# Optimization experiments

Measured on AMD Instinct MI355X. Metric: run time of the kernel, lower is better.

Reference implementation:

```python
import jax, jax.numpy as jnp
import numpy as np

B, C, H, W = 2, 48, 128, 256
HEADS = 3
EPS_LN = 1e-6
EPS_NRM = 1e-12


def _conv(x, w, b, padding=0, dilation=1, groups=1):
    # x: NCHW, w: OIHW
    out = jax.lax.conv_general_dilated(
        x, w, window_strides=(1, 1),
        padding=[(padding, padding), (padding, padding)],
        rhs_dilation=(dilation, dilation),
        feature_group_count=groups,
        dimension_numbers=('NCHW', 'OIHW', 'NCHW'))
    return out + b[None, :, None, None]


def _ln2d(x, w, b):
    # LayerNorm over channel dim per pixel (NAFNet-style LayerNorm2d)
    mu = x.mean(axis=1, keepdims=True)
    var = ((x - mu) ** 2).mean(axis=1, keepdims=True)
    return (x - mu) / jnp.sqrt(var + EPS_LN) * w[None, :, None, None] + b[None, :, None, None]


def _l2norm(x):
    # F.normalize(dim=-1): x / max(||x||_2, eps)
    n = jnp.sqrt((x * x).sum(-1, keepdims=True))
    return x / jnp.maximum(n, EPS_NRM)


def setup_inputs() -> dict:
    key = jax.random.key(0)
    ks = iter(jax.random.split(key, 40))
    def nrm(shape, s=0.02):
        return jax.random.normal(next(ks), shape, jnp.float32) * s
    d = {
        'x_l': jax.random.normal(next(ks), (B, C, H, W), jnp.float32),
        'x_r': jax.random.normal(next(ks), (B, C, H, W), jnp.float32),
        'ln1_w': jnp.ones((C,), jnp.float32), 'ln1_b': jnp.zeros((C,), jnp.float32),
        'ln2_w': jnp.ones((C,), jnp.float32), 'ln2_b': jnp.zeros((C,), jnp.float32),
        'qkv_l_w': nrm((3 * C, C, 1, 1)), 'qkv_l_b': jnp.zeros((3 * C,), jnp.float32),
        'qkv_r_w': nrm((3 * C, C, 1, 1)), 'qkv_r_b': jnp.zeros((3 * C,), jnp.float32),
        'dw_l_w': nrm((3 * C, 1, 3, 3)), 'dw_l_b': jnp.zeros((3 * C,), jnp.float32),
        'dw_r_w': nrm((3 * C, 1, 3, 3)), 'dw_r_b': jnp.zeros((3 * C,), jnp.float32),
        'dil0_w': nrm((2 * C, 2 * C, 3, 3)), 'dil0_b': jnp.zeros((2 * C,), jnp.float32),
        'dil1_w': nrm((2 * C, 2 * C, 3, 3)), 'dil1_b': jnp.zeros((2 * C,), jnp.float32),
        'dil2_w': nrm((2 * C, 2 * C, 3, 3)), 'dil2_b': jnp.zeros((2 * C,), jnp.float32),
        'convQ_w': nrm((C, 6 * C, 1, 1)), 'convQ_b': jnp.zeros((C,), jnp.float32),
        'conv1_w': nrm((C, C, 1, 1)), 'conv1_b': jnp.zeros((C,), jnp.float32),
        'conv2_w': nrm((C, C, 1, 1)), 'conv2_b': jnp.zeros((C,), jnp.float32),
        'temperature': jnp.ones((HEADS, 1, 1), jnp.float32),
    }
    return d


def reference(x_l, x_r, ln1_w, ln1_b, ln2_w, ln2_b,
              qkv_l_w, qkv_l_b, qkv_r_w, qkv_r_b,
              dw_l_w, dw_l_b, dw_r_w, dw_r_b,
              dil0_w, dil0_b, dil1_w, dil1_b, dil2_w, dil2_b,
              convQ_w, convQ_b, conv1_w, conv1_b, conv2_w, conv2_b,
              temperature):
    b, c, h, w = x_l.shape
    hw = h * w
    ch = c // HEADS  # channels per head

    norm_l = _ln2d(x_l, ln1_w, ln1_b)
    norm_r = _ln2d(x_r, ln2_w, ln2_b)

    qkvl = _conv(_conv(norm_l, qkv_l_w, qkv_l_b), dw_l_w, dw_l_b, padding=1, groups=3 * c)
    qkvr = _conv(_conv(norm_r, qkv_r_w, qkv_r_b), dw_r_w, dw_r_b, padding=1, groups=3 * c)
    Q_l, K_l, V_l = jnp.split(qkvl, 3, axis=1)
    Q_r, K_r, V_r = jnp.split(qkvr, 3, axis=1)

    Q = jnp.concatenate((Q_l, Q_r), axis=1)  # [b, 2c, h, w]
    Q = jnp.concatenate((
        _conv(Q, dil0_w, dil0_b, padding=2, dilation=2),
        _conv(Q, dil1_w, dil1_b, padding=4, dilation=4),
        _conv(Q, dil2_w, dil2_b, padding=6, dilation=6)), axis=1)  # [b, 6c, h, w]
    Q = _conv(Q, convQ_w, convQ_b)  # [b, c, h, w]

    def heads(t):
        return t.reshape(b, HEADS, ch, hw)

    Q = _l2norm(heads(Q))
    K_l = _l2norm(heads(K_l))
    K_r = _l2norm(heads(K_r))
    V_l = heads(V_l)
    V_r = heads(V_r)

    # channel attention: [b, head, ch, ch]
    A_r2l = jax.nn.softmax(jnp.einsum('bhcn,bhdn->bhcd', Q, K_r) * temperature, axis=-1)
    A_l2r = jax.nn.softmax(jnp.einsum('bhcn,bhdn->bhcd', Q, K_l) * temperature, axis=-1)

    F_l = jnp.einsum('bhcd,bhdn->bhcn', A_r2l, V_l).reshape(b, c, h, w)
    F_r = jnp.einsum('bhcd,bhdn->bhcn', A_l2r, V_r).reshape(b, c, h, w)

    F_l = _conv(F_l, conv1_w, conv1_b)
    F_r = _conv(F_r, conv2_w, conv2_b)
    return (x_l + F_l, x_r + F_r)
```

## Files before the change

### kernel.cpp

```cpp
#include <hip/hip_runtime.h>
#include <hip/hip_bf16.h>

typedef __hip_bfloat16 bf16;
typedef __attribute__((ext_vector_type(8))) short short8;
typedef __attribute__((ext_vector_type(4))) float f32x4;

constexpr int IMG_H = 128;
constexpr int IMG_W = 256;
constexpr int HW    = IMG_H * IMG_W;
constexpr int BB    = 2;
constexpr int CC    = 48;
constexpr int C3    = 144;
constexpr int XPW   = 268;
constexpr int XOFF  = 6;

constexpr int WO_QKVL_W = 0;
constexpr int WO_QKVR_W = 6912;
constexpr int WO_DWL_W  = 13824;
constexpr int WO_DWR_W  = 15120;
constexpr int WO_C1_W   = 16416;
constexpr int WO_C2_W   = 18720;
constexpr int WO_QKVL_B = 21024;
constexpr int WO_QKVR_B = 21168;
constexpr int WO_DWL_B  = 21312;
constexpr int WO_DWR_B  = 21456;
constexpr int WO_C1_B   = 21600;
constexpr int WO_C2_B   = 21648;
constexpr int WO_LN1W   = 21696;
constexpr int WO_LN1B   = 21744;
constexpr int WO_LN2W   = 21792;
constexpr int WO_LN2B   = 21840;
constexpr int WO_TEMP   = 21888;
constexpr int WO_WQ     = 21952;
constexpr int WO_D0W    = 35776;
constexpr int WO_D1W    = 118720;
constexpr int WO_D2W    = 201664;
constexpr int WO_BQ     = 284608;
constexpr int WO_B0     = 284656;
constexpr int WO_B1     = 284752;
constexpr int WO_B2     = 284848;
constexpr int WO_WPACK  = 284944;
constexpr int WO_EFFB   = 409360;
constexpr int WO_NQ     = 409424;
constexpr int WO_NKL    = 409520;
constexpr int WO_NKR    = 409616;
constexpr int WO_AR2L   = 409712;
constexpr int WO_AL2R   = 411248;
constexpr int WO_M1     = 412800;
constexpr int WO_M2     = 417408;
constexpr int WO_WQP    = 422016;
constexpr int WO_PART   = 431232;

constexpr size_t ACT_BASE_BYTES = 2118144;

constexpr size_t A_P  = 0;
constexpr size_t A_Q1 = 9437184;
constexpr size_t A_Q2 = 18874368;
constexpr size_t A_QC = 28311552;

struct PrepArgs {
  const void* src[25];
  int dst[25];
  int n[25];
};

__device__ __forceinline__ bool probe_bf16(const void* ln1w) {
  return ((const unsigned short*)ln1w)[0] == 0x3F80;
}

__global__ __launch_bounds__(256) void prep_k(PrepArgs a, float* __restrict__ wsf) {
  bool isb = probe_bf16(a.src[12]);
  int t = blockIdx.y;
  int i = blockIdx.x * 256 + threadIdx.x;
  if (i < a.n[t]) {
    float v = isb ? __bfloat162float(((const bf16*)a.src[t])[i])
                  : ((const float*)a.src[t])[i];
    wsf[a.dst[t] + i] = v;
  }
}

__global__ __launch_bounds__(256) void effw2_k(const float* __restrict__ wsf,
                                               bf16* __restrict__ wpack) {
  int d  = blockIdx.x / 96;
  int ci = blockIdx.x % 96;
  __shared__ float wds[864];
  __shared__ float wqs[48 * 97];
  const int wdb = (d == 0) ? WO_D0W : (d == 1) ? WO_D1W : WO_D2W;
  for (int idx = threadIdx.x; idx < 864; idx += 256) {
    int m = idx / 9, tt = idx % 9;
    wds[idx] = wsf[wdb + (m * 96 + ci) * 9 + tt];
  }
  for (int idx = threadIdx.x; idx < 4608; idx += 256) {
    int co = idx / 96, m = idx % 96;
    wqs[co * 97 + m] = wsf[WO_WQ + co * 288 + d * 96 + m];
  }
  __syncthreads();
  int tco = threadIdx.x;
  if (tco < 432) {
    int t = tco / 48, co = tco % 48;
    float s = 0.f;
#pragma unroll 8
    for (int m = 0; m < 96; ++m) s += wqs[co * 97 + m] * wds[m * 9 + t];
    int kc = ci >> 5, j = ci & 7;
    int L = ((ci & 31) >> 3) * 16 + (co & 15);
    int nt = co >> 4;
    int f = ((d * 9 + t) * 3 + kc) * 3 + nt;
    wpack[(size_t)f * 512 + L * 8 + j] = __float2bfloat16(s);
  }
}

__global__ __launch_bounds__(64) void effb_k(const float* __restrict__ wsf,
                                             float* __restrict__ effb) {
  int co = threadIdx.x;
  if (co >= 48) return;
  float s = wsf[WO_BQ + co];
  for (int m = 0; m < 96; ++m) {
    s += wsf[WO_WQ + co * 288 + m]       * wsf[WO_B0 + m];
    s += wsf[WO_WQ + co * 288 + 96 + m]  * wsf[WO_B1 + m];
    s += wsf[WO_WQ + co * 288 + 192 + m] * wsf[WO_B2 + m];
  }
  effb[co] = s;
}

__global__ __launch_bounds__(256) void wqp_k(const float* __restrict__ wsf,
                                             bf16* __restrict__ wqp) {
  int idx = blockIdx.x * 256 + threadIdx.x;
  if (idx >= 18432) return;
  int side = idx / 9216;
  int rem = idx % 9216;
  int nt = rem / 1024;
  int kt = (rem / 512) % 2;
  int e  = rem % 512;
  int L = e >> 3, j = e & 7;
  int o = nt * 16 + (L & 15);
  int kp = kt * 32 + (L >> 4) * 8 + j;
  int g = kp >> 4, r = kp & 15;
  float val = 0.f;
  if (r < 12) {
    int c = g * 12 + r;
    val = wsf[(side ? WO_QKVR_W : WO_QKVL_W) + o * 48 + c];
  }
  wqp[idx] = __float2bfloat16(val);
}

__global__ __launch_bounds__(256) void ln_k(
    const void* __restrict__ x, const void* __restrict__ probe,
    const float* __restrict__ lnw, const float* __restrict__ lnb,
    bf16* __restrict__ xn) {
  int px = threadIdx.x & 63;
  int w  = threadIdx.x >> 6;
  int p  = blockIdx.x * 64 + px;
  int b  = p >> 15;
  int pix = p & (HW - 1);
  size_t base = (size_t)b * CC * HW + pix;
  float v[12];
  if (probe_bf16(probe)) {
    const bf16* xp = (const bf16*)x + base;
#pragma unroll
    for (int c = 0; c < 12; ++c)
      v[c] = __bfloat162float(xp[(size_t)(w * 12 + c) * HW]);
  } else {
    const float* xp = (const float*)x + base;
#pragma unroll
    for (int c = 0; c < 12; ++c) v[c] = xp[(size_t)(w * 12 + c) * HW];
  }
  float s = 0.f, s2 = 0.f;
#pragma unroll
  for (int c = 0; c < 12; ++c) { s += v[c]; s2 += v[c] * v[c]; }
  __shared__ float2 red[4][64];
  red[w][px] = make_float2(s, s2);
  __syncthreads();
  float S = 0.f, S2 = 0.f;
#pragma unroll
  for (int i = 0; i < 4; ++i) { S += red[i][px].x; S2 += red[i][px].y; }
  float mu = S * (1.f / 48.f);
  float var = S2 * (1.f / 48.f) - mu * mu;
  float rs = rsqrtf(var + 1e-6f);
  bf16 o[16];
#pragma unroll
  for (int c = 0; c < 12; ++c)
    o[c] = __float2bfloat16((v[c] - mu) * rs * lnw[w * 12 + c] + lnb[w * 12 + c]);
#pragma unroll
  for (int c = 12; c < 16; ++c) o[c] = __float2bfloat16(0.f);
  bf16* dst = xn + (size_t)p * 64 + w * 16;
  *(uint4*)(dst) = *(uint4*)(o);
  *(uint4*)(dst + 8) = *(uint4*)(o + 8);
}

__global__ __launch_bounds__(256) void qkv_mfma_k(
    const bf16* __restrict__ xn, const bf16* __restrict__ wqp_side,
    const float* __restrict__ qb, bf16* __restrict__ pre) {
  __shared__ __align__(16) bf16 W[18 * 512];
  __shared__ __align__(16) bf16 Cs[144][72];
  for (int i = threadIdx.x; i < 1152; i += 256)
    ((uint4*)W)[i] = ((const uint4*)wqp_side)[i];
  __syncthreads();
  int L = threadIdx.x & 63, w = threadIdx.x >> 6;
  int lo = L & 15, hi = L >> 4;
  int p0 = blockIdx.x * 64 + w * 16;
  const bf16* abase = xn + (size_t)(p0 + lo) * 64 + hi * 8;
  short8 a0 = *(const short8*)(abase);
  short8 a1 = *(const short8*)(abase + 32);
#pragma unroll
  for (int nt = 0; nt < 9; ++nt) {
    float bv = qb[nt * 16 + lo];
    f32x4 acc = {bv, bv, bv, bv};
    acc = __builtin_amdgcn_mfma_f32_16x16x32_bf16(
        a0, *(const short8*)(W + (nt * 2 + 0) * 512 + L * 8), acc, 0, 0, 0);
    acc = __builtin_amdgcn_mfma_f32_16x16x32_bf16(
        a1, *(const short8*)(W + (nt * 2 + 1) * 512 + L * 8), acc, 0, 0, 0);
#pragma unroll
    for (int r = 0; r < 4; ++r)
      Cs[nt * 16 + lo][w * 16 + hi * 4 + r] = __float2bfloat16(acc[r]);
  }
  __syncthreads();
  int b = (blockIdx.x * 64) >> 15;
  int pix0 = (blockIdx.x * 64) & (HW - 1);
#pragma unroll
  for (int pass = 0; pass < 18; ++pass) {
    int o = pass * 8 + (threadIdx.x >> 5);
    int px = (threadIdx.x & 31) * 2;
    bf16 t2[2];
    t2[0] = Cs[o][px];
    t2[1] = Cs[o][px + 1];
    *(unsigned*)(pre + ((size_t)(b * C3 + o)) * HW + pix0 + px) = *(unsigned*)t2;
  }
}

__global__ __launch_bounds__(256) void dw_k(
    const bf16* __restrict__ in, const float* __restrict__ w9,
    const float* __restrict__ bias, bf16* __restrict__ out) {
  int gid = blockIdx.x;
  int yt = gid & 15;
  int c = (gid >> 4) % C3;
  int b = gid / (16 * C3);
  int ry = threadIdx.x >> 5, xi = threadIdx.x & 31;
  int y = yt * 8 + ry;
  int x0 = xi * 8;
  const bf16* base = in + ((size_t)(b * C3 + c)) * HW;
  float wv[9];
#pragma unroll
  for (int t = 0; t < 9; ++t) wv[t] = w9[c * 9 + t];
  float bz = bias[c];
  float acc[8];
#pragma unroll
  for (int i = 0; i < 8; ++i) acc[i] = bz;
#pragma unroll
  for (int ky = 0; ky < 3; ++ky) {
    int yy = y + ky - 1;
    if ((unsigned)yy >= (unsigned)IMG_H) continue;
    const bf16* row = base + yy * IMG_W + x0;
    uint4 m = *(const uint4*)(row);
    float f[10];
    f[0] = (x0 > 0) ? __bfloat162float(row[-1]) : 0.f;
    f[9] = (x0 + 8 < IMG_W) ? __bfloat162float(row[8]) : 0.f;
    f[1] = __uint_as_float(m.x << 16);
    f[2] = __uint_as_float(m.x & 0xFFFF0000u);
    f[3] = __uint_as_float(m.y << 16);
    f[4] = __uint_as_float(m.y & 0xFFFF0000u);
    f[5] = __uint_as_float(m.z << 16);
    f[6] = __uint_as_float(m.z & 0xFFFF0000u);
    f[7] = __uint_as_float(m.w << 16);
    f[8] = __uint_as_float(m.w & 0xFFFF0000u);
    float w0 = wv[ky * 3], w1 = wv[ky * 3 + 1], w2 = wv[ky * 3 + 2];
#pragma unroll
    for (int i = 0; i < 8; ++i)
      acc[i] += w0 * f[i] + w1 * f[i + 1] + w2 * f[i + 2];
  }
  bf16 o[8];
#pragma unroll
  for (int i = 0; i < 8; ++i) o[i] = __float2bfloat16(acc[i]);
  *(uint4*)(out + ((size_t)(b * C3 + c)) * HW + y * IMG_W + x0) = *(uint4*)o;
}

__global__ __launch_bounds__(256) void qc_k(const bf16* __restrict__ q1,
                                            const bf16* __restrict__ q2,
                                            bf16* __restrict__ qc) {
  int b = blockIdx.x >> 7;
  int y = blockIdx.x & 127;
  int half = blockIdx.y;
  int tid = threadIdx.x;
  int x0 = half * 128;
  int px = tid & 127;
  int cig = tid >> 7;
  __shared__ __align__(16) bf16 T[128][100];
#pragma unroll 8
  for (int k = 0; k < 48; ++k) {
    int ci = cig * 48 + k;
    const bf16* src = (ci < 48)
        ? q1 + (((size_t)(b * C3 + ci)) * IMG_H + y) * IMG_W
        : q2 + (((size_t)(b * C3 + ci - 48)) * IMG_H + y) * IMG_W;
    T[px][ci] = src[x0 + px];
  }
  __syncthreads();
  size_t rowbase = ((size_t)(b * IMG_H + y)) * XPW * 96 + (size_t)half * 12864;
#pragma unroll 1
  for (int i = 0; i < 13; ++i) {
    int e4 = i * 256 + tid;
    if (e4 >= 3216) break;
    int e = e4 * 4;
    int xp = (e + half * 12864) / 96;
    int ci = (e + half * 12864) % 96;
    int x = xp - XOFF;
    uint2 val;
    if ((unsigned)x < (unsigned)IMG_W) {
      val = *(const uint2*)(&T[x - x0][ci]);
    } else {
      val.x = 0u; val.y = 0u;
    }
    *(uint2*)(qc + rowbase + e) = val;
  }
}

__global__ __launch_bounds__(256) void dil_mfma_k(
    const bf16* __restrict__ qc, const bf16* __restrict__ wp,
    const float* __restrict__ effb, bf16* __restrict__ qh) {
  __shared__ __align__(16) unsigned char LDSU[26304];
  bf16* Wb = (bf16*)LDSU;
  float* Cs = (float*)LDSU;
  int tid = threadIdx.x;
  int L = tid & 63;
  int w = tid >> 6;
  int lo = L & 15, hi = L >> 4;
  int x0 = blockIdx.x * 128;
  int y = blockIdx.y;
  int b = blockIdx.z;

  f32x4 acc[2][3];
#pragma unroll
  for (int s = 0; s < 2; ++s)
#pragma unroll
    for (int nt = 0; nt < 3; ++nt) {
      float bv = effb[nt * 16 + lo];
      acc[s][nt] = {bv, bv, bv, bv};
    }

  const size_t abase =
      ((size_t)(b * IMG_H + y) * XPW + XOFF + x0 + w * 32 + lo) * 96 + hi * 8;

  {
    const uint4* src = (const uint4*)(wp);
    uint4* dst = (uint4*)(Wb);
    dst[tid] = src[tid];
    dst[tid + 256] = src[tid + 256];
    if (tid < 64) dst[tid + 512] = src[tid + 512];
  }
  __syncthreads();

#pragma unroll 1
  for (int ti = 0; ti < 27; ++ti) {
    if (ti + 1 < 27) {
      const uint4* src = (const uint4*)(wp + (ti + 1) * 4608);
      uint4* dst = (uint4*)(Wb + ((ti + 1) & 1) * 4608);
      dst[tid] = src[tid];
      dst[tid + 256] = src[tid + 256];
      if (tid < 64) dst[tid + 512] = src[tid + 512];
    }
    int d = ti / 9, t = ti - d * 9;
    int D = 2 * (d + 1);
    int dy = (t / 3 - 1) * D;
    int dx = (t % 3 - 1) * D;
    int yy = y + dy;
    if ((unsigned)yy < (unsigned)IMG_H) {
      const bf16* wb = Wb + (ti & 1) * 4608 + L * 8;
      const bf16* ap = qc + abase + ((long)dy * XPW + dx) * 96;
#pragma unroll
      for (int kc = 0; kc < 3; ++kc) {
        short8 a0 = *(const short8*)(ap + kc * 32);
        short8 a1 = *(const short8*)(ap + kc * 32 + 1536);
        const bf16* wk = wb + kc * 3 * 512;
#pragma unroll
        for (int nt = 0; nt < 3; ++nt) {
          short8 wv = *(const short8*)(wk + nt * 512);
          acc[0][nt] = __builtin_amdgcn_mfma_f32_16x16x32_bf16(
              a0, wv, acc[0][nt], 0, 0, 0);
          acc[1][nt] = __builtin_amdgcn_mfma_f32_16x16x32_bf16(
              a1, wv, acc[1][nt], 0, 0, 0);
        }
      }
    }
    __syncthreads();
  }

#pragma unroll
  for (int s = 0; s < 2; ++s)
#pragma unroll
    for (int nt = 0; nt < 3; ++nt)
#pragma unroll
      for (int r = 0; r < 4; ++r)
        Cs[(nt * 16 + lo) * 137 + w * 32 + s * 16 + hi * 4 + r] = acc[s][nt][r];
  __syncthreads();
#pragma unroll
  for (int it = 0; it < 3; ++it) {
    int e = (it * 256 + tid) * 8;
    int co = e >> 7;
    int px = e & 127;
    const float* srcp = &Cs[co * 137 + px];
    bf16 tmp[8];
#pragma unroll
    for (int i2 = 0; i2 < 8; ++i2) tmp[i2] = __float2bfloat16(srcp[i2]);
    *(uint4*)(qh + (((size_t)(b * CC + co)) * IMG_H + y) * IMG_W + x0 + px) =
        *(uint4*)tmp;
  }
}

__device__ __forceinline__ float wave_sum(float v) {
#pragma unroll
  for (int off = 32; off > 0; off >>= 1) v += __shfl_down(v, off, 64);
  return v;
}

__device__ __forceinline__ float blo(unsigned u) {
  return __uint_as_float(u << 16);
}
__device__ __forceinline__ float bhi(unsigned u) {
  return __uint_as_float(u & 0xFFFF0000u);
}

__global__ __launch_bounds__(256) void rownorm_k(
    const bf16* __restrict__ qh, const bf16* __restrict__ qkvl,
    const bf16* __restrict__ qkvr, float* __restrict__ nq,
    float* __restrict__ nkl, float* __restrict__ nkr) {
  int id = blockIdx.x;
  int which = id / 96;
  int rid = id % 96;
  int b = rid / 48;
  int c = rid % 48;
  const bf16* ptr = (which == 0) ? qh + ((size_t)(b * CC + c)) * HW
                  : (which == 1) ? qkvl + ((size_t)(b * C3 + 48 + c)) * HW
                                 : qkvr + ((size_t)(b * C3 + 48 + c)) * HW;
  float s = 0.f;
#pragma unroll 2
  for (int it = 0; it < 16; ++it) {
    int n0 = (it * 256 + threadIdx.x) * 8;
    uint4 u = *(const uint4*)(ptr + n0);
    float a0 = blo(u.x), a1 = bhi(u.x), a2 = blo(u.y), a3 = bhi(u.y);
    float a4 = blo(u.z), a5 = bhi(u.z), a6 = blo(u.w), a7 = bhi(u.w);
    s += a0 * a0 + a1 * a1 + a2 * a2 + a3 * a3 + a4 * a4 + a5 * a5 +
         a6 * a6 + a7 * a7;
  }
  s = wave_sum(s);
  __shared__ float red[4];
  if ((threadIdx.x & 63) == 0) red[threadIdx.x >> 6] = s;
  __syncthreads();
  if (threadIdx.x == 0) {
    float tot = red[0] + red[1] + red[2] + red[3];
    float* dst = (which == 0) ? nq : (which == 1) ? nkl : nkr;
    dst[rid] = tot;
  }
}

__global__ __launch_bounds__(256) void logits_mfma_k(
    const bf16* __restrict__ qh, const bf16* __restrict__ qkvl,
    const bf16* __restrict__ qkvr, float* __restrict__ part) {
  int abh = blockIdx.x;
  int chunk = blockIdx.y;
  int a = abh / 6;
  int b = (abh / 3) % 2;
  int h = abh % 3;
  int tid = threadIdx.x;
  int L = tid & 63, w = tid >> 6;
  int lo = L & 15, hi = L >> 4;
  const bf16* qrow = qh + ((size_t)(b * CC + h * 16 + lo)) * HW;
  const bf16* krow =
      ((a == 0) ? qkvr : qkvl) + ((size_t)(b * C3 + 48 + h * 16 + lo)) * HW;
  int px0 = chunk * 1024 + w * 256 + hi * 8;
  f32x4 acc = {0.f, 0.f, 0.f, 0.f};
#pragma unroll
  for (int s = 0; s < 8; ++s) {
    short8 av = *(const short8*)(qrow + px0 + s * 32);
    short8 bv = *(const short8*)(krow + px0 + s * 32);
    acc = __builtin_amdgcn_mfma_f32_16x16x32_bf16(av, bv, acc, 0, 0, 0);
  }
  __shared__ float red[4][256];
#pragma unroll
  for (int r = 0; r < 4; ++r) red[w][(hi * 4 + r) * 16 + lo] = acc[r];
  __syncthreads();
  float sum = red[0][tid] + red[1][tid] + red[2][tid] + red[3][tid];
  part[((size_t)abh * 32 + chunk) * 256 + tid] = sum;
}

__global__ __launch_bounds__(256) void logits_red_k(
    const float* __restrict__ part, const float* __restrict__ nq,
    const float* __restrict__ nkl, const float* __restrict__ nkr,
    const float* __restrict__ temp, float* __restrict__ logr2l,
    float* __restrict__ logl2r) {
  int abh = blockIdx.x;
  int a = abh / 6, b = (abh / 3) % 2, h = abh % 3;
  int t = threadIdx.x;
  int i = t >> 4, j = t & 15;
  float s = 0.f;
  const float* p = part + (size_t)abh * 32 * 256 + t;
#pragma unroll 8
  for (int c = 0; c < 32; ++c) s += p[c * 256];
  float qn = fmaxf(sqrtf(nq[b * 48 + h * 16 + i]), 1e-12f);
  float kn = fmaxf(sqrtf(((a == 0) ? nkr : nkl)[b * 48 + h * 16 + j]), 1e-12f);
  float val = s / (qn * kn) * temp[h];
  ((a == 0) ? logr2l : logl2r)[b * 768 + h * 256 + i * 16 + j] = val;
}

__global__ __launch_bounds__(256) void softmaxM_k(float* __restrict__ wsf) {
  int tid = threadIdx.x;
  __shared__ float A1[1536], A2[1536];
  if (tid < 192) {
    const float* p = wsf + ((tid < 96) ? WO_AR2L : WO_AL2R) + (tid % 96) * 16;
    float* dst = ((tid < 96) ? A1 : A2) + (tid % 96) * 16;
    float m = -1e30f;
#pragma unroll
    for (int j = 0; j < 16; ++j) m = fmaxf(m, p[j]);
    float s = 0.f;
    float e[16];
#pragma unroll
    for (int j = 0; j < 16; ++j) {
      e[j] = expf(p[j] - m);
      s += e[j];
    }
    float inv = 1.f / s;
#pragma unroll
    for (int j = 0; j < 16; ++j) dst[j] = e[j] * inv;
  }
  __syncthreads();
#pragma unroll 1
  for (int idx = tid; idx < 4608; idx += 256) {
    int b = idx / 2304;
    int r = idx % 2304;
    int o = r / 48;
    int cp = r % 48;
    int h = cp >> 4, j = cp & 15;
    const float* a1 = &A1[((b * 3 + h) * 16) * 16 + j];
    const float* a2 = &A2[((b * 3 + h) * 16) * 16 + j];
    float s1 = 0.f, s2 = 0.f;
#pragma unroll
    for (int i = 0; i < 16; ++i) {
      s1 += wsf[WO_C1_W + o * 48 + h * 16 + i] * a1[i * 16];
      s2 += wsf[WO_C2_W + o * 48 + h * 16 + i] * a2[i * 16];
    }
    wsf[WO_M1 + idx] = s1;
    wsf[WO_M2 + idx] = s2;
  }
}

__global__ __launch_bounds__(256) void attn_out2_k(
    const bf16* __restrict__ qkv, const void* __restrict__ x,
    const void* __restrict__ probe, const float* __restrict__ M,
    const float* __restrict__ cb, void* __restrict__ out, int half) {
  int tid = threadIdx.x;
  int p = blockIdx.x * 256 + tid;
  int b = __builtin_amdgcn_readfirstlane(p >> 15);
  int pix = p & (HW - 1);
  int o0 = blockIdx.y * 16;
  bool isb = probe_bf16(probe);

  float v[CC];
  const bf16* vb = qkv + ((size_t)(b * C3 + 96)) * HW + pix;
#pragma unroll
  for (int c = 0; c < CC; ++c) v[c] = __bfloat162float(vb[(size_t)c * HW]);

  const float* Mb = M + b * 2304;
  size_t base = (size_t)b * CC * HW + pix;
  float res[16];
#pragma unroll 2
  for (int o = 0; o < 16; ++o) {
    float acc = cb[o0 + o];
    const float* mrow = Mb + (o0 + o) * 48;
#pragma unroll
    for (int c = 0; c < CC; ++c) acc += mrow[c] * v[c];
    res[o] = acc;
  }
  size_t obase = (size_t)half * BB * CC * HW + base + (size_t)o0 * HW;
  if (isb) {
    const bf16* xp = (const bf16*)x + base + (size_t)o0 * HW;
    bf16* op = (bf16*)out + obase;
#pragma unroll
    for (int o = 0; o < 16; ++o)
      op[(size_t)o * HW] =
          __float2bfloat16(res[o] + __bfloat162float(xp[(size_t)o * HW]));
  } else {
    const float* xp = (const float*)x + base + (size_t)o0 * HW;
    float* op = (float*)out + obase;
#pragma unroll
    for (int o = 0; o < 16; ++o) op[(size_t)o * HW] = res[o] + xp[(size_t)o * HW];
  }
}

extern "C" void kernel_launch(void* const* d_in, const int* in_sizes, int n_in,
                              void* d_out, int out_size, void* d_ws, size_t ws_size,
                              hipStream_t stream) {
  (void)in_sizes; (void)n_in; (void)out_size; (void)ws_size;
  const void* x_l = d_in[0];
  const void* x_r = d_in[1];
  const void* probe = d_in[2];
  float* wsf = (float*)d_ws;
  bf16* wpack = (bf16*)(wsf + WO_WPACK);
  bf16* wqp = (bf16*)(wsf + WO_WQP);
  bf16* act = (bf16*)((char*)d_ws + ACT_BASE_BYTES);
  bf16* P  = act + A_P;
  bf16* Q1 = act + A_Q1;
  bf16* Q2 = act + A_Q2;
  bf16* QC = act + A_QC;
  bf16* XN = act + A_QC;
  bf16* qh = P;

  PrepArgs pa;
  const int srcIdx[25] = {6, 8, 10, 12, 22, 24, 7, 9, 11, 13, 23, 25,
                          2, 3, 4, 5, 26, 20, 14, 16, 18, 21, 15, 17, 19};
  const int dstOff[25] = {WO_QKVL_W, WO_QKVR_W, WO_DWL_W, WO_DWR_W, WO_C1_W, WO_C2_W,
                          WO_QKVL_B, WO_QKVR_B, WO_DWL_B, WO_DWR_B, WO_C1_B, WO_C2_B,
                          WO_LN1W, WO_LN1B, WO_LN2W, WO_LN2B, WO_TEMP,
                          WO_WQ, WO_D0W, WO_D1W, WO_D2W, WO_BQ, WO_B0, WO_B1, WO_B2};
  const int ns[25] = {6912, 6912, 1296, 1296, 2304, 2304, 144, 144, 144, 144,
                      48, 48, 48, 48, 48, 48, 3,
                      13824, 82944, 82944, 82944, 48, 96, 96, 96};
  for (int i = 0; i < 25; ++i) {
    pa.src[i] = d_in[srcIdx[i]];
    pa.dst[i] = dstOff[i];
    pa.n[i] = ns[i];
  }
  prep_k<<<dim3(324, 25), 256, 0, stream>>>(pa, wsf);

  effw2_k<<<288, 256, 0, stream>>>(wsf, wpack);
  effb_k<<<1, 64, 0, stream>>>(wsf, wsf + WO_EFFB);
  wqp_k<<<72, 256, 0, stream>>>(wsf, wqp);

  ln_k<<<1024, 256, 0, stream>>>(x_l, probe, wsf + WO_LN1W, wsf + WO_LN1B, XN);
  qkv_mfma_k<<<1024, 256, 0, stream>>>(XN, wqp, wsf + WO_QKVL_B, P);
  dw_k<<<BB * C3 * 16, 256, 0, stream>>>(P, wsf + WO_DWL_W, wsf + WO_DWL_B, Q1);
  ln_k<<<1024, 256, 0, stream>>>(x_r, probe, wsf + WO_LN2W, wsf + WO_LN2B, XN);
  qkv_mfma_k<<<1024, 256, 0, stream>>>(XN, wqp + 9216, wsf + WO_QKVR_B, P);
  dw_k<<<BB * C3 * 16, 256, 0, stream>>>(P, wsf + WO_DWR_W, wsf + WO_DWR_B, Q2);

  qc_k<<<dim3(BB * IMG_H, 2), 256, 0, stream>>>(Q1, Q2, QC);

  dil_mfma_k<<<dim3(IMG_W / 128, IMG_H, BB), 256, 0, stream>>>(
      QC, wpack, wsf + WO_EFFB, qh);

  rownorm_k<<<288, 256, 0, stream>>>(qh, Q1, Q2, wsf + WO_NQ,
                                     wsf + WO_NKL, wsf + WO_NKR);
  logits_mfma_k<<<dim3(12, 32), 256, 0, stream>>>(qh, Q1, Q2, wsf + WO_PART);
  logits_red_k<<<12, 256, 0, stream>>>(wsf + WO_PART, wsf + WO_NQ,
                                       wsf + WO_NKL, wsf + WO_NKR,
                                       wsf + WO_TEMP, wsf + WO_AR2L,
                                       wsf + WO_AL2R);
  softmaxM_k<<<1, 256, 0, stream>>>(wsf);

  attn_out2_k<<<dim3(256, 3), 256, 0, stream>>>(
      Q1, x_l, probe, wsf + WO_M1, wsf + WO_C1_B, d_out, 0);
  attn_out2_k<<<dim3(256, 3), 256, 0, stream>>>(
      Q2, x_r, probe, wsf + WO_M2, wsf + WO_C2_B, d_out, 1);
}
```

Baseline: 294.0 us.

## Fuse layernorm into QKV MFMA, re-tile dilated conv by channel group, merge attn_out launches

```diff
diff --git a/kernel.cpp b/kernel.cpp
--- a/kernel.cpp
+++ b/kernel.cpp
@@ -101,10 +101,14 @@
     float s = 0.f;
 #pragma unroll 8
     for (int m = 0; m < 96; ++m) s += wqs[co * 97 + m] * wds[m * 9 + t];
+    int trow = t / 3, dxi = t % 3;
+    int ti = (trow == 0) ? (2 - d) * 3 + dxi
+           : (trow == 1) ? 9 + d * 3 + dxi
+                         : 18 + d * 3 + dxi;
     int kc = ci >> 5, j = ci & 7;
     int L = ((ci & 31) >> 3) * 16 + (co & 15);
     int nt = co >> 4;
-    int f = ((d * 9 + t) * 3 + kc) * 3 + nt;
+    int f = (ti * 3 + kc) * 3 + nt;
     wpack[(size_t)f * 512 + L * 8 + j] = __float2bfloat16(s);
   }
 }
@@ -143,14 +147,24 @@
   wqp[idx] = __float2bfloat16(val);
 }
 
-__global__ __launch_bounds__(256) void ln_k(
+__global__ __launch_bounds__(256) void lnqkv_k(
     const void* __restrict__ x, const void* __restrict__ probe,
     const float* __restrict__ lnw, const float* __restrict__ lnb,
-    bf16* __restrict__ xn) {
-  int px = threadIdx.x & 63;
-  int w  = threadIdx.x >> 6;
-  int p  = blockIdx.x * 64 + px;
-  int b  = p >> 15;
+    const bf16* __restrict__ wqp_side, const float* __restrict__ qb,
+    bf16* __restrict__ pre) {
+  __shared__ __align__(16) unsigned char LDSU[21504 + 18432];
+  bf16* XNs = (bf16*)LDSU;
+  float2* red = (float2*)(LDSU + 9216);
+  bf16* Cs = (bf16*)LDSU;
+  bf16* W = (bf16*)(LDSU + 21504);
+  int tid = threadIdx.x;
+  for (int i = tid; i < 1152; i += 256)
+    ((uint4*)W)[i] = ((const uint4*)wqp_side)[i];
+
+  int px = tid & 63;
+  int w = tid >> 6;
+  int p = blockIdx.x * 64 + px;
+  int b = p >> 15;
   int pix = p & (HW - 1);
   size_t base = (size_t)b * CC * HW + pix;
   float v[12];
@@ -167,63 +181,55 @@
   float s = 0.f, s2 = 0.f;
 #pragma unroll
   for (int c = 0; c < 12; ++c) { s += v[c]; s2 += v[c] * v[c]; }
-  __shared__ float2 red[4][64];
-  red[w][px] = make_float2(s, s2);
+  red[w * 64 + px] = make_float2(s, s2);
   __syncthreads();
   float S = 0.f, S2 = 0.f;
 #pragma unroll
-  for (int i = 0; i < 4; ++i) { S += red[i][px].x; S2 += red[i][px].y; }
+  for (int i = 0; i < 4; ++i) {
+    float2 r2 = red[i * 64 + px];
+    S += r2.x; S2 += r2.y;
+  }
   float mu = S * (1.f / 48.f);
   float var = S2 * (1.f / 48.f) - mu * mu;
   float rs = rsqrtf(var + 1e-6f);
-  bf16 o[16];
+  bf16 o16[16];
 #pragma unroll
   for (int c = 0; c < 12; ++c)
-    o[c] = __float2bfloat16((v[c] - mu) * rs * lnw[w * 12 + c] + lnb[w * 12 + c]);
-#pragma unroll
-  for (int c = 12; c < 16; ++c) o[c] = __float2bfloat16(0.f);
-  bf16* dst = xn + (size_t)p * 64 + w * 16;
-  *(uint4*)(dst) = *(uint4*)(o);
-  *(uint4*)(dst + 8) = *(uint4*)(o + 8);
-}
-
-__global__ __launch_bounds__(256) void qkv_mfma_k(
-    const bf16* __restrict__ xn, const bf16* __restrict__ wqp_side,
-    const float* __restrict__ qb, bf16* __restrict__ pre) {
-  __shared__ __align__(16) bf16 W[18 * 512];
-  __shared__ __align__(16) bf16 Cs[144][72];
-  for (int i = threadIdx.x; i < 1152; i += 256)
-    ((uint4*)W)[i] = ((const uint4*)wqp_side)[i];
-  __syncthreads();
-  int L = threadIdx.x & 63, w = threadIdx.x >> 6;
+    o16[c] = __float2bfloat16((v[c] - mu) * rs * lnw[w * 12 + c] + lnb[w * 12 + c]);
+#pragma unroll
+  for (int c = 12; c < 16; ++c) o16[c] = __float2bfloat16(0.f);
+  *(uint4*)(XNs + px * 72 + w * 16) = *(uint4*)(o16);
+  *(uint4*)(XNs + px * 72 + w * 16 + 8) = *(uint4*)(o16 + 8);
+  __syncthreads();
+
+  int L = tid & 63;
   int lo = L & 15, hi = L >> 4;
-  int p0 = blockIdx.x * 64 + w * 16;
-  const bf16* abase = xn + (size_t)(p0 + lo) * 64 + hi * 8;
-  short8 a0 = *(const short8*)(abase);
-  short8 a1 = *(const short8*)(abase + 32);
+  const bf16* arow = XNs + (size_t)(w * 16 + lo) * 72 + hi * 8;
+  short8 a0 = *(const short8*)(arow);
+  short8 a1 = *(const short8*)(arow + 32);
+  __syncthreads();
 #pragma unroll
   for (int nt = 0; nt < 9; ++nt) {
-    float bv = qb[nt * 16 + lo];
-    f32x4 acc = {bv, bv, bv, bv};
+    float bvv = qb[nt * 16 + lo];
+    f32x4 acc = {bvv, bvv, bvv, bvv};
     acc = __builtin_amdgcn_mfma_f32_16x16x32_bf16(
         a0, *(const short8*)(W + (nt * 2 + 0) * 512 + L * 8), acc, 0, 0, 0);
     acc = __builtin_amdgcn_mfma_f32_16x16x32_bf16(
         a1, *(const short8*)(W + (nt * 2 + 1) * 512 + L * 8), acc, 0, 0, 0);
 #pragma unroll
     for (int r = 0; r < 4; ++r)
-      Cs[nt * 16 + lo][w * 16 + hi * 4 + r] = __float2bfloat16(acc[r]);
-  }
-  __syncthreads();
-  int b = (blockIdx.x * 64) >> 15;
+      Cs[(nt * 16 + lo) * 66 + w * 16 + hi * 4 + r] = __float2bfloat16(acc[r]);
+  }
+  __syncthreads();
   int pix0 = (blockIdx.x * 64) & (HW - 1);
 #pragma unroll
   for (int pass = 0; pass < 18; ++pass) {
-    int o = pass * 8 + (threadIdx.x >> 5);
-    int px = (threadIdx.x & 31) * 2;
+    int o = pass * 8 + (tid >> 5);
+    int px2 = (tid & 31) * 2;
     bf16 t2[2];
-    t2[0] = Cs[o][px];
-    t2[1] = Cs[o][px + 1];
-    *(unsigned*)(pre + ((size_t)(b * C3 + o)) * HW + pix0 + px) = *(unsigned*)t2;
+    t2[0] = Cs[o * 66 + px2];
+    t2[1] = Cs[o * 66 + px2 + 1];
+    *(unsigned*)(pre + ((size_t)(b * C3 + o)) * HW + pix0 + px2) = *(unsigned*)t2;
   }
 }
 
@@ -312,70 +318,66 @@
   }
 }
 
-__global__ __launch_bounds__(256) void dil_mfma_k(
+__global__ __launch_bounds__(128) void dil_mfma_k(
     const bf16* __restrict__ qc, const bf16* __restrict__ wp,
     const float* __restrict__ effb, bf16* __restrict__ qh) {
-  __shared__ __align__(16) unsigned char LDSU[26304];
+  __shared__ __align__(16) unsigned char LDSU[8768];
   bf16* Wb = (bf16*)LDSU;
   float* Cs = (float*)LDSU;
+  int bid = blockIdx.x;
+  int xcd = bid & 7;
+  int slot = bid >> 3;
+  int y = xcd * 16 + (slot & 15);
+  int rest = slot >> 4;
+  int xt = rest & 1;
+  int b = (rest >> 1) & 1;
+  int cg = rest >> 2;
   int tid = threadIdx.x;
   int L = tid & 63;
   int w = tid >> 6;
   int lo = L & 15, hi = L >> 4;
-  int x0 = blockIdx.x * 128;
-  int y = blockIdx.y;
-  int b = blockIdx.z;
-
-  f32x4 acc[2][3];
-#pragma unroll
-  for (int s = 0; s < 2; ++s)
-#pragma unroll
-    for (int nt = 0; nt < 3; ++nt) {
-      float bv = effb[nt * 16 + lo];
-      acc[s][nt] = {bv, bv, bv, bv};
-    }
-
+  int x0 = xt * 128;
+
+  f32x4 acc[4];
+  {
+    float bv = effb[cg * 16 + lo];
+#pragma unroll
+    for (int s = 0; s < 4; ++s) acc[s] = {bv, bv, bv, bv};
+  }
   const size_t abase =
-      ((size_t)(b * IMG_H + y) * XPW + XOFF + x0 + w * 32 + lo) * 96 + hi * 8;
-
-  {
-    const uint4* src = (const uint4*)(wp);
-    uint4* dst = (uint4*)(Wb);
-    dst[tid] = src[tid];
-    dst[tid + 256] = src[tid + 256];
-    if (tid < 64) dst[tid + 512] = src[tid + 512];
+      ((size_t)(b * IMG_H + y) * XPW + XOFF + x0 + w * 64 + lo) * 96 + hi * 8;
+
+  for (int t = tid; t < 192; t += 128) {
+    int kc = t >> 6, e = t & 63;
+    ((uint4*)(Wb))[kc * 64 + e] =
+        *((const uint4*)(wp + ((size_t)(0 * 3 + kc) * 3 + cg) * 512) + e);
   }
   __syncthreads();
 
 #pragma unroll 1
   for (int ti = 0; ti < 27; ++ti) {
     if (ti + 1 < 27) {
-      const uint4* src = (const uint4*)(wp + (ti + 1) * 4608);
-      uint4* dst = (uint4*)(Wb + ((ti + 1) & 1) * 4608);
-      dst[tid] = src[tid];
-      dst[tid + 256] = src[tid + 256];
-      if (tid < 64) dst[tid + 512] = src[tid + 512];
+      int tn = ti + 1;
+      for (int t = tid; t < 192; t += 128) {
+        int kc = t >> 6, e = t & 63;
+        ((uint4*)(Wb + (tn & 1) * 1536))[kc * 64 + e] =
+            *((const uint4*)(wp + ((size_t)(tn * 3 + kc) * 3 + cg) * 512) + e);
+      }
     }
-    int d = ti / 9, t = ti - d * 9;
-    int D = 2 * (d + 1);
-    int dy = (t / 3 - 1) * D;
-    int dx = (t % 3 - 1) * D;
-    int yy = y + dy;
-    if ((unsigned)yy < (unsigned)IMG_H) {
-      const bf16* wb = Wb + (ti & 1) * 4608 + L * 8;
+    int g = ti / 3, dxi = ti - g * 3;
+    int D = (g < 3) ? (6 - 2 * g) : (g < 6) ? (2 * (g - 2)) : (2 * (g - 5));
+    int dy = (g < 3) ? -D : (g < 6) ? 0 : D;
+    int dx = (dxi - 1) * D;
+    if ((unsigned)(y + dy) < (unsigned)IMG_H) {
+      const bf16* wb = Wb + (ti & 1) * 1536;
       const bf16* ap = qc + abase + ((long)dy * XPW + dx) * 96;
 #pragma unroll
       for (int kc = 0; kc < 3; ++kc) {
-        short8 a0 = *(const short8*)(ap + kc * 32);
-        short8 a1 = *(const short8*)(ap + kc * 32 + 1536);
-        const bf16* wk = wb + kc * 3 * 512;
-#pragma unroll
-        for (int nt = 0; nt < 3; ++nt) {
-          short8 wv = *(const short8*)(wk + nt * 512);
-          acc[0][nt] = __builtin_amdgcn_mfma_f32_16x16x32_bf16(
-              a0, wv, acc[0][nt], 0, 0, 0);
-          acc[1][nt] = __builtin_amdgcn_mfma_f32_16x16x32_bf16(
-              a1, wv, acc[1][nt], 0, 0, 0);
+        short8 wv = *(const short8*)(wb + kc * 512 + L * 8);
+#pragma unroll
+        for (int s = 0; s < 4; ++s) {
+          short8 a = *(const short8*)(ap + kc * 32 + s * 1536);
+          acc[s] = __builtin_amdgcn_mfma_f32_16x16x32_bf16(a, wv, acc[s], 0, 0, 0);
         }
       }
     }
@@ -383,24 +385,22 @@
   }
 
 #pragma unroll
-  for (int s = 0; s < 2; ++s)
-#pragma unroll
-    for (int nt = 0; nt < 3; ++nt)
-#pragma unroll
-      for (int r = 0; r < 4; ++r)
-        Cs[(nt * 16 + lo) * 137 + w * 32 + s * 16 + hi * 4 + r] = acc[s][nt][r];
-  __syncthreads();
-#pragma unroll
-  for (int it = 0; it < 3; ++it) {
-    int e = (it * 256 + tid) * 8;
+  for (int s = 0; s < 4; ++s)
+#pragma unroll
+    for (int r = 0; r < 4; ++r)
+      Cs[lo * 137 + w * 64 + s * 16 + hi * 4 + r] = acc[s][r];
+  __syncthreads();
+#pragma unroll
+  for (int p = 0; p < 2; ++p) {
+    int e = (p * 128 + tid) * 8;
     int co = e >> 7;
     int px = e & 127;
     const float* srcp = &Cs[co * 137 + px];
     bf16 tmp[8];
 #pragma unroll
     for (int i2 = 0; i2 < 8; ++i2) tmp[i2] = __float2bfloat16(srcp[i2]);
-    *(uint4*)(qh + (((size_t)(b * CC + co)) * IMG_H + y) * IMG_W + x0 + px) =
-        *(uint4*)tmp;
+    *(uint4*)(qh + (((size_t)(b * CC + cg * 16 + co)) * IMG_H + y) * IMG_W +
+              x0 + px) = *(uint4*)tmp;
   }
 }
 
@@ -541,9 +541,15 @@
 }
 
 __global__ __launch_bounds__(256) void attn_out2_k(
-    const bf16* __restrict__ qkv, const void* __restrict__ x,
-    const void* __restrict__ probe, const float* __restrict__ M,
-    const float* __restrict__ cb, void* __restrict__ out, int half) {
+    const bf16* __restrict__ q1, const bf16* __restrict__ q2,
+    const void* __restrict__ x1, const void* __restrict__ x2,
+    const void* __restrict__ probe, const float* __restrict__ Mall,
+    const float* __restrict__ cball, void* __restrict__ out) {
+  int side = blockIdx.z;
+  const bf16* qkv = side ? q2 : q1;
+  const void* x = side ? x2 : x1;
+  const float* M = Mall + side * 4608;
+  const float* cb = cball + side * 48;
   int tid = threadIdx.x;
   int p = blockIdx.x * 256 + tid;
   int b = __builtin_amdgcn_readfirstlane(p >> 15);
@@ -567,7 +573,7 @@
     for (int c = 0; c < CC; ++c) acc += mrow[c] * v[c];
     res[o] = acc;
   }
-  size_t obase = (size_t)half * BB * CC * HW + base + (size_t)o0 * HW;
+  size_t obase = (size_t)side * BB * CC * HW + base + (size_t)o0 * HW;
   if (isb) {
     const bf16* xp = (const bf16*)x + base + (size_t)o0 * HW;
     bf16* op = (bf16*)out + obase;
@@ -598,7 +604,6 @@
   bf16* Q1 = act + A_Q1;
   bf16* Q2 = act + A_Q2;
   bf16* QC = act + A_QC;
-  bf16* XN = act + A_QC;
   bf16* qh = P;
 
   PrepArgs pa;
@@ -622,17 +627,16 @@
   effb_k<<<1, 64, 0, stream>>>(wsf, wsf + WO_EFFB);
   wqp_k<<<72, 256, 0, stream>>>(wsf, wqp);
 
-  ln_k<<<1024, 256, 0, stream>>>(x_l, probe, wsf + WO_LN1W, wsf + WO_LN1B, XN);
-  qkv_mfma_k<<<1024, 256, 0, stream>>>(XN, wqp, wsf + WO_QKVL_B, P);
+  lnqkv_k<<<1024, 256, 0, stream>>>(x_l, probe, wsf + WO_LN1W, wsf + WO_LN1B,
+                                    wqp, wsf + WO_QKVL_B, P);
   dw_k<<<BB * C3 * 16, 256, 0, stream>>>(P, wsf + WO_DWL_W, wsf + WO_DWL_B, Q1);
-  ln_k<<<1024, 256, 0, stream>>>(x_r, probe, wsf + WO_LN2W, wsf + WO_LN2B, XN);
-  qkv_mfma_k<<<1024, 256, 0, stream>>>(XN, wqp + 9216, wsf + WO_QKVR_B, P);
+  lnqkv_k<<<1024, 256, 0, stream>>>(x_r, probe, wsf + WO_LN2W, wsf + WO_LN2B,
+                                    wqp + 9216, wsf + WO_QKVR_B, P);
   dw_k<<<BB * C3 * 16, 256, 0, stream>>>(P, wsf + WO_DWR_W, wsf + WO_DWR_B, Q2);
 
   qc_k<<<dim3(BB * IMG_H, 2), 256, 0, stream>>>(Q1, Q2, QC);
 
-  dil_mfma_k<<<dim3(IMG_W / 128, IMG_H, BB), 256, 0, stream>>>(
-      QC, wpack, wsf + WO_EFFB, qh);
+  dil_mfma_k<<<1536, 128, 0, stream>>>(QC, wpack, wsf + WO_EFFB, qh);
 
   rownorm_k<<<288, 256, 0, stream>>>(qh, Q1, Q2, wsf + WO_NQ,
                                      wsf + WO_NKL, wsf + WO_NKR);
@@ -643,8 +647,6 @@
                                        wsf + WO_AL2R);
   softmaxM_k<<<1, 256, 0, stream>>>(wsf);
 
-  attn_out2_k<<<dim3(256, 3), 256, 0, stream>>>(
-      Q1, x_l, probe, wsf + WO_M1, wsf + WO_C1_B, d_out, 0);
-  attn_out2_k<<<dim3(256, 3), 256, 0, stream>>>(
-      Q2, x_r, probe, wsf + WO_M2, wsf + WO_C2_B, d_out, 1);
-}
+  attn_out2_k<<<dim3(256, 3, 2), 256, 0, stream>>>(
+      Q1, Q2, x_l, x_r, probe, wsf + WO_M1, wsf + WO_C1_B, d_out);
+}
```

After: 315.2 us. 1.07x slower.
